# Optimization experiments

Hardware: AMD Instinct MI355X
Metric: run time of the kernel (lower is better)

## Reference

```python
import jax, jax.numpy as jnp
import numpy as np

T, B, DIM, N = 2048, 16, 1024, 64


def setup_inputs() -> dict:
    key = jax.random.key(0)
    ks = jax.random.split(key, 6)
    # xavier-uniform-ish scale for [N, DIM] linear weights
    lim = float(np.sqrt(6.0 / (DIM + N)))
    mk = lambda k: jax.random.uniform(k, (N, DIM), jnp.float32, -lim, lim)
    return {
        "x": jax.random.normal(ks[0], (T, B, DIM), jnp.float32),
        "S": jnp.zeros((B, N, N), jnp.float32),
        "W_k": mk(ks[1]),
        "W_v": mk(ks[2]),
        "W_q": mk(ks[3]),
        "W_alpha": mk(ks[4]),
        "d_alpha": jnp.full((N,), 0.1, jnp.float32),
        "b_alpha": jnp.full((N,), 2.0, jnp.float32),
    }


def reference(x, S, W_k, W_v, W_q, W_alpha, d_alpha, b_alpha):
    # Projections for the whole sequence at once: [T, B, N]
    k_all = jnp.einsum('tbd,nd->tbn', x, W_k)
    v_all = jnp.einsum('tbd,nd->tbn', x, W_v)
    q_all = jnp.einsum('tbd,nd->tbn', x, W_q)
    a_all = jnp.einsum('tbd,nd->tbn', x, W_alpha)

    def step(S, inp):
        k, v, q, ax = inp  # each [B, N]
        retrieved = jnp.einsum('bij,bj->bi', S, k)                 # [B, N]
        alpha = jax.nn.sigmoid(ax + d_alpha * retrieved + b_alpha)  # [B, N]
        outer_vk = v[:, :, None] * k[:, None, :]                    # [B, N, N]
        S = alpha[:, :, None] * S + (1.0 - alpha[:, :, None]) * outer_vk
        out = jnp.einsum('bij,bj->bi', S, q)                        # [B, N]
        out = out * jax.nn.silu(out)
        return S, out

    S_final, output = jax.lax.scan(step, S, (k_all, v_all, q_all, a_all))
    return output, S_final
```

## Files before the change

kernel.cpp:

```cpp
#include <hip/hip_runtime.h>
#include <hip/hip_bf16.h>

#define T_STEPS 2048
#define BATCH 16
#define DIM 1024
#define NDIM 64
#define M_TOTAL (T_STEPS * BATCH)
#define STRIDE (BATCH * NDIM)
#define CH 32

typedef __attribute__((ext_vector_type(8))) short bf16x8;
typedef __attribute__((ext_vector_type(4))) float f32x4;

__device__ inline unsigned pk_bf(float lo, float hi) {
    __hip_bfloat162 h = __float22bfloat162_rn(float2{lo, hi});
    return *(unsigned*)&h;
}

template <int CTRL>
__device__ inline float dpp_add(float x) {
    int v = __builtin_amdgcn_update_dpp(0, __float_as_int(x), CTRL, 0xF, 0xF, true);
    return x + __int_as_float(v);
}
__device__ inline float red16(float x) {
    x = dpp_add<0xB1>(x);
    x = dpp_add<0x4E>(x);
    x = dpp_add<0x141>(x);
    x = dpp_add<0x140>(x);
    return x;
}
__device__ inline float fast_sigmoid(float z) {
    return __builtin_amdgcn_rcpf(1.f + __expf(-z));
}

#define AS1 __attribute__((address_space(1)))
#define AS3 __attribute__((address_space(3)))
__device__ inline void gl_lds16(const float* g, float* l) {
    __builtin_amdgcn_global_load_lds((const AS1 unsigned*)g, (AS3 unsigned*)l, 16, 0, 0);
}
__device__ inline void gl_lds4(const float* g, float* l) {
    __builtin_amdgcn_global_load_lds((const AS1 unsigned*)g, (AS3 unsigned*)l, 4, 0, 0);
}
#define WAIT_VM0 do { __builtin_amdgcn_s_waitcnt(0x0F70); asm volatile("" ::: "memory"); } while (0)

__global__ __launch_bounds__(256, 2) void proj_kernel(
    const float* __restrict__ x,
    const float* __restrict__ Wk, const float* __restrict__ Wv,
    const float* __restrict__ Wq, const float* __restrict__ Wa,
    const float* __restrict__ ba,
    float* __restrict__ outBase, float* __restrict__ kqOut) {
    const int LDA = 40;
    __shared__ unsigned short lA[64 * 40];
    __shared__ unsigned short lB[256 * 40];

    int m0 = blockIdx.x * 64;
    int tid = threadIdx.x;
    int wave = tid >> 6;
    int lane = tid & 63;
    int lrow = lane & 15;
    int quad = lane >> 4;

    f32x4 acc[16];
#pragma unroll
    for (int b = 0; b < 16; b++) acc[b] = (f32x4)(0.f);

    int arow = tid >> 2;
    int acol = (tid & 3) * 8;
    int widx = tid >> 6;
    const float* Wsel = (widx == 0) ? Wk : (widx == 1) ? Wv : (widx == 2) ? Wq : Wa;
    const float* wrow = Wsel + (size_t)(tid & 63) * DIM;
    const float* xrow = x + (size_t)(m0 + arow) * DIM + acol;

    float4 a0 = ((const float4*)xrow)[0], a1 = ((const float4*)xrow)[1];
    float4 bb[8];
#pragma unroll
    for (int jj = 0; jj < 8; jj++) bb[jj] = ((const float4*)wrow)[jj];
    unsigned apk[4], bpk[16];
    apk[0] = pk_bf(a0.x, a0.y); apk[1] = pk_bf(a0.z, a0.w);
    apk[2] = pk_bf(a1.x, a1.y); apk[3] = pk_bf(a1.z, a1.w);
#pragma unroll
    for (int jj = 0; jj < 8; jj++) {
        bpk[2 * jj] = pk_bf(bb[jj].x, bb[jj].y);
        bpk[2 * jj + 1] = pk_bf(bb[jj].z, bb[jj].w);
    }

    for (int k0 = 0; k0 < DIM; k0 += 32) {
        __syncthreads();
        *(uint4*)&lA[arow * LDA + acol] = *(uint4*)&apk[0];
        *(uint4*)&lB[tid * LDA + 0]  = *(uint4*)&bpk[0];
        *(uint4*)&lB[tid * LDA + 8]  = *(uint4*)&bpk[4];
        *(uint4*)&lB[tid * LDA + 16] = *(uint4*)&bpk[8];
        *(uint4*)&lB[tid * LDA + 24] = *(uint4*)&bpk[12];
        __syncthreads();

        bool more = (k0 + 32) < DIM;
        float4 na0, na1, nb[8];
        if (more) {
            const float4* pa = (const float4*)(xrow + k0 + 32);
            na0 = pa[0]; na1 = pa[1];
            const float4* pb = (const float4*)(wrow + k0 + 32);
#pragma unroll
            for (int jj = 0; jj < 8; jj++) nb[jj] = pb[jj];
        }

        bf16x8 af = *(const bf16x8*)&lA[(wave * 16 + lrow) * LDA + quad * 8];
#pragma unroll
        for (int bt = 0; bt < 16; bt++) {
            bf16x8 bfr = *(const bf16x8*)&lB[(bt * 16 + lrow) * LDA + quad * 8];
            acc[bt] = __builtin_amdgcn_mfma_f32_16x16x32_bf16(af, bfr, acc[bt], 0, 0, 0);
        }

        if (more) {
            apk[0] = pk_bf(na0.x, na0.y); apk[1] = pk_bf(na0.z, na0.w);
            apk[2] = pk_bf(na1.x, na1.y); apk[3] = pk_bf(na1.z, na1.w);
#pragma unroll
            for (int jj = 0; jj < 8; jj++) {
                bpk[2 * jj] = pk_bf(nb[jj].x, nb[jj].y);
                bpk[2 * jj + 1] = pk_bf(nb[jj].z, nb[jj].w);
            }
        }
    }

#pragma unroll
    for (int bt = 12; bt < 16; bt++) {
        float bav = ba[(bt - 12) * 16 + lrow];
#pragma unroll
        for (int reg = 0; reg < 4; reg++) acc[bt][reg] += bav;
    }
    const size_t per = (size_t)M_TOTAL * NDIM;
#pragma unroll
    for (int bt = 0; bt < 16; bt++) {
        int n = bt * 16 + lrow;
        float* outW = outBase + (size_t)(n >> 6) * per + (n & 63);
#pragma unroll
        for (int reg = 0; reg < 4; reg++) {
            int m = m0 + wave * 16 + quad * 4 + reg;
            outW[(size_t)m * NDIM] = acc[bt][reg];
        }
    }
#pragma unroll
    for (int reg = 0; reg < 4; reg++) {
        float p = acc[0][reg] * acc[8][reg] + acc[1][reg] * acc[9][reg] +
                  acc[2][reg] * acc[10][reg] + acc[3][reg] * acc[11][reg];
        p = red16(p);
        if (lrow == 0) kqOut[m0 + wave * 16 + quad * 4 + reg] = p;
    }
}

__global__ __launch_bounds__(64, 1) void recur_kernel(
    const float* __restrict__ Kp, const float* __restrict__ Vp,
    const float* __restrict__ Qp, const float* __restrict__ Ap,
    const float* __restrict__ KQp, const float* __restrict__ S0,
    const float* __restrict__ d_alpha, float* __restrict__ out,
    float* __restrict__ Sout) {
    __shared__ float Kl[2][CH][64];
    __shared__ float Ql[2][CH][64];
    __shared__ float VAl[2][CH][8];
    __shared__ float KQl[2][64];

    int b = blockIdx.y;
    int g = blockIdx.x;
    int lane = threadIdx.x;
    int r = lane >> 4;
    int c = lane & 15;
    int i = g * 4 + r;
    int c4 = c * 4;

    float4 s = *(const float4*)(S0 + ((size_t)b * NDIM + i) * NDIM + c4);
    float da = d_alpha[i];

    const float* Kbase = Kp + (size_t)b * NDIM + (size_t)(lane >> 4) * STRIDE + (lane & 15) * 4;
    const float* Qbase = Qp + (size_t)b * NDIM + (size_t)(lane >> 4) * STRIDE + (lane & 15) * 4;
    const float* VAbase = ((lane & 1) ? Ap : Vp) + (size_t)b * NDIM + g * 4 + (size_t)(lane >> 1) * STRIDE;
    const float* KQbase = KQp + b + (size_t)(lane & 31) * BATCH;

    auto load_chunk = [&](int t0, int buf) {
#pragma unroll
        for (int j = 0; j < 8; ++j) {
            gl_lds16(Kbase + (size_t)(t0 + j * 4) * STRIDE, &Kl[buf][j * 4][0]);
            gl_lds16(Qbase + (size_t)(t0 + j * 4) * STRIDE, &Ql[buf][j * 4][0]);
        }
        gl_lds16(VAbase + (size_t)t0 * STRIDE, &VAl[buf][0][0]);
        gl_lds4(KQbase + (size_t)t0 * BATCH, &KQl[buf][0]);
    };

    load_chunk(0, 0);
    WAIT_VM0;

    float* ob = out + (size_t)b * NDIM + i;

    for (int j = 0; j < T_STEPS / CH; ++j) {
        int cb = j & 1;
        if (j < T_STEPS / CH - 1) load_chunk((j + 1) * CH, cb ^ 1);

        const float* Kb = &Kl[cb][0][0];
        const float* Qb = &Ql[cb][0][0];
        const float* Vb = &VAl[cb][0][0];
        const float* Qk = &KQl[cb][0];

        float4 kr[2], qr[2];
        float vr[2], ar[2], kqr[2];
#pragma unroll
        for (int u = 0; u < 2; ++u) {
            kr[u] = *(const float4*)(Kb + u * 64 + c4);
            qr[u] = *(const float4*)(Qb + u * 64 + c4);
            vr[u] = Vb[u * 8 + r];
            ar[u] = Vb[u * 8 + 4 + r];
            kqr[u] = Qk[u];
        }

#pragma unroll
        for (int tl = 0; tl < CH; ++tl) {
            int sl = tl & 1;
            float4 k = kr[sl], q = qr[sl];
            float v = vr[sl], aa = ar[sl], kq = kqr[sl];
            if (tl < CH - 2) {
                kr[sl] = *(const float4*)(Kb + (tl + 2) * 64 + c4);
                qr[sl] = *(const float4*)(Qb + (tl + 2) * 64 + c4);
                vr[sl] = Vb[(tl + 2) * 8 + r];
                ar[sl] = Vb[(tl + 2) * 8 + 4 + r];
                kqr[sl] = Qk[tl + 2];
            }

            float rk = fmaf(k.y, s.y, k.x * s.x) + fmaf(k.w, s.w, k.z * s.z);
            float rq = fmaf(q.y, s.y, q.x * s.x) + fmaf(q.w, s.w, q.z * s.z);
            rk = red16(rk);
            rq = red16(rq);

            float z = fmaf(da, rk, aa);
            float alpha = fast_sigmoid(z);
            float u1 = (1.f - alpha) * v;

            s.x = fmaf(alpha, s.x, u1 * k.x);
            s.y = fmaf(alpha, s.y, u1 * k.y);
            s.z = fmaf(alpha, s.z, u1 * k.z);
            s.w = fmaf(alpha, s.w, u1 * k.w);

            float o = fmaf(alpha, rq, u1 * kq);
            float ov = o * o * fast_sigmoid(o);
            if (c == 0) ob[(size_t)(j * CH + tl) * STRIDE] = ov;
        }
        WAIT_VM0;
    }

    *(float4*)(Sout + ((size_t)b * NDIM + i) * NDIM + c4) = s;
}

extern "C" void kernel_launch(void* const* d_in, const int* in_sizes, int n_in,
                              void* d_out, int out_size, void* d_ws, size_t ws_size,
                              hipStream_t stream) {
    const float* x  = (const float*)d_in[0];
    const float* S0 = (const float*)d_in[1];
    const float* Wk = (const float*)d_in[2];
    const float* Wv = (const float*)d_in[3];
    const float* Wq = (const float*)d_in[4];
    const float* Wa = (const float*)d_in[5];
    const float* da = (const float*)d_in[6];
    const float* ba = (const float*)d_in[7];

    float* out = (float*)d_out;
    float* Sout = out + (size_t)T_STEPS * BATCH * NDIM;

    float* proj = (float*)d_ws;
    const size_t per = (size_t)M_TOTAL * NDIM;
    float* Kp = proj;
    float* Vp = proj + per;
    float* Qp = proj + 2 * per;
    float* Ap = proj + 3 * per;
    float* kq = proj + 4 * per;

    proj_kernel<<<dim3(M_TOTAL / 64), dim3(256), 0, stream>>>(x, Wk, Wv, Wq, Wa, ba, proj, kq);
    recur_kernel<<<dim3(16, BATCH), dim3(64), 0, stream>>>(Kp, Vp, Qp, Ap, kq, S0, da, out, Sout);
}
```

Baseline: 546.8 us.

## Prepack weights to bf16, drop LDS in projection GEMM, widen recurrence rows per lane

Adds a pre-pass that converts the four weight matrices to bf16 once per call. The projection GEMM then reads A and B fragments straight from global memory, with no LDS staging and no barriers, and each wave computes two 16-row tiles that share the same B fragments. The recurrence kernel now gives each lane 8 state columns instead of 4, which halves the block count, shortens the DPP reduction to 8 lanes, and uses packed float2 math for the state update. The trade is more global traffic and less latency hiding in the GEMM, and more serial work per lane in the recurrence, in exchange for fewer reduction steps and fewer barriers.

```diff
diff --git a/kernel.cpp b/kernel.cpp
--- a/kernel.cpp
+++ b/kernel.cpp
@@ -11,6 +11,7 @@
 
 typedef __attribute__((ext_vector_type(8))) short bf16x8;
 typedef __attribute__((ext_vector_type(4))) float f32x4;
+typedef __attribute__((ext_vector_type(2))) float f32x2;
 
 __device__ inline unsigned pk_bf(float lo, float hi) {
     __hip_bfloat162 h = __float22bfloat162_rn(float2{lo, hi});
@@ -29,6 +30,12 @@
     x = dpp_add<0x140>(x);
     return x;
 }
+__device__ inline float red8(float x) {
+    x = dpp_add<0xB1>(x);
+    x = dpp_add<0x4E>(x);
+    x = dpp_add<0x141>(x);
+    return x;
+}
 __device__ inline float fast_sigmoid(float z) {
     return __builtin_amdgcn_rcpf(1.f + __expf(-z));
 }
@@ -43,81 +50,59 @@
 }
 #define WAIT_VM0 do { __builtin_amdgcn_s_waitcnt(0x0F70); asm volatile("" ::: "memory"); } while (0)
 
-__global__ __launch_bounds__(256, 2) void proj_kernel(
-    const float* __restrict__ x,
+__global__ __launch_bounds__(256) void pack_w(
     const float* __restrict__ Wk, const float* __restrict__ Wv,
     const float* __restrict__ Wq, const float* __restrict__ Wa,
+    unsigned short* __restrict__ Wb) {
+    int n = blockIdx.x;
+    int sel = n >> 6;
+    const float* W = (sel == 0) ? Wk : (sel == 1) ? Wv : (sel == 2) ? Wq : Wa;
+    int k4 = threadIdx.x * 4;
+    float4 f = *(const float4*)(W + (size_t)(n & 63) * DIM + k4);
+    uint2 u;
+    u.x = pk_bf(f.x, f.y);
+    u.y = pk_bf(f.z, f.w);
+    *(uint2*)(Wb + (size_t)n * DIM + k4) = u;
+}
+
+__global__ __launch_bounds__(256, 2) void proj_kernel(
+    const float* __restrict__ x, const unsigned short* __restrict__ Wb,
     const float* __restrict__ ba,
     float* __restrict__ outBase, float* __restrict__ kqOut) {
-    const int LDA = 40;
-    __shared__ unsigned short lA[64 * 40];
-    __shared__ unsigned short lB[256 * 40];
-
-    int m0 = blockIdx.x * 64;
     int tid = threadIdx.x;
-    int wave = tid >> 6;
+    int wv = tid >> 6;
     int lane = tid & 63;
     int lrow = lane & 15;
     int quad = lane >> 4;
-
-    f32x4 acc[16];
-#pragma unroll
-    for (int b = 0; b < 16; b++) acc[b] = (f32x4)(0.f);
-
-    int arow = tid >> 2;
-    int acol = (tid & 3) * 8;
-    int widx = tid >> 6;
-    const float* Wsel = (widx == 0) ? Wk : (widx == 1) ? Wv : (widx == 2) ? Wq : Wa;
-    const float* wrow = Wsel + (size_t)(tid & 63) * DIM;
-    const float* xrow = x + (size_t)(m0 + arow) * DIM + acol;
-
-    float4 a0 = ((const float4*)xrow)[0], a1 = ((const float4*)xrow)[1];
-    float4 bb[8];
-#pragma unroll
-    for (int jj = 0; jj < 8; jj++) bb[jj] = ((const float4*)wrow)[jj];
-    unsigned apk[4], bpk[16];
-    apk[0] = pk_bf(a0.x, a0.y); apk[1] = pk_bf(a0.z, a0.w);
-    apk[2] = pk_bf(a1.x, a1.y); apk[3] = pk_bf(a1.z, a1.w);
-#pragma unroll
-    for (int jj = 0; jj < 8; jj++) {
-        bpk[2 * jj] = pk_bf(bb[jj].x, bb[jj].y);
-        bpk[2 * jj + 1] = pk_bf(bb[jj].z, bb[jj].w);
-    }
+    int m0 = blockIdx.x * 128 + wv * 32;
+
+    f32x4 acc[2][16];
+#pragma unroll
+    for (int a = 0; a < 2; a++)
+#pragma unroll
+        for (int b = 0; b < 16; b++) acc[a][b] = (f32x4)(0.f);
+
+    const float* xr0 = x + (size_t)(m0 + lrow) * DIM + quad * 8;
+    const float* xr1 = xr0 + (size_t)16 * DIM;
+    const unsigned short* wb = Wb + (size_t)lrow * DIM + quad * 8;
 
     for (int k0 = 0; k0 < DIM; k0 += 32) {
-        __syncthreads();
-        *(uint4*)&lA[arow * LDA + acol] = *(uint4*)&apk[0];
-        *(uint4*)&lB[tid * LDA + 0]  = *(uint4*)&bpk[0];
-        *(uint4*)&lB[tid * LDA + 8]  = *(uint4*)&bpk[4];
-        *(uint4*)&lB[tid * LDA + 16] = *(uint4*)&bpk[8];
-        *(uint4*)&lB[tid * LDA + 24] = *(uint4*)&bpk[12];
-        __syncthreads();
-
-        bool more = (k0 + 32) < DIM;
-        float4 na0, na1, nb[8];
-        if (more) {
-            const float4* pa = (const float4*)(xrow + k0 + 32);
-            na0 = pa[0]; na1 = pa[1];
-            const float4* pb = (const float4*)(wrow + k0 + 32);
-#pragma unroll
-            for (int jj = 0; jj < 8; jj++) nb[jj] = pb[jj];
-        }
-
-        bf16x8 af = *(const bf16x8*)&lA[(wave * 16 + lrow) * LDA + quad * 8];
+        float4 a00 = ((const float4*)(xr0 + k0))[0];
+        float4 a01 = ((const float4*)(xr0 + k0))[1];
+        float4 a10 = ((const float4*)(xr1 + k0))[0];
+        float4 a11 = ((const float4*)(xr1 + k0))[1];
+        unsigned p0[4], p1[4];
+        p0[0] = pk_bf(a00.x, a00.y); p0[1] = pk_bf(a00.z, a00.w);
+        p0[2] = pk_bf(a01.x, a01.y); p0[3] = pk_bf(a01.z, a01.w);
+        p1[0] = pk_bf(a10.x, a10.y); p1[1] = pk_bf(a10.z, a10.w);
+        p1[2] = pk_bf(a11.x, a11.y); p1[3] = pk_bf(a11.z, a11.w);
+        bf16x8 af0 = *(bf16x8*)&p0[0];
+        bf16x8 af1 = *(bf16x8*)&p1[0];
 #pragma unroll
         for (int bt = 0; bt < 16; bt++) {
-            bf16x8 bfr = *(const bf16x8*)&lB[(bt * 16 + lrow) * LDA + quad * 8];
-            acc[bt] = __builtin_amdgcn_mfma_f32_16x16x32_bf16(af, bfr, acc[bt], 0, 0, 0);
-        }
-
-        if (more) {
-            apk[0] = pk_bf(na0.x, na0.y); apk[1] = pk_bf(na0.z, na0.w);
-            apk[2] = pk_bf(na1.x, na1.y); apk[3] = pk_bf(na1.z, na1.w);
-#pragma unroll
-            for (int jj = 0; jj < 8; jj++) {
-                bpk[2 * jj] = pk_bf(nb[jj].x, nb[jj].y);
-                bpk[2 * jj + 1] = pk_bf(nb[jj].z, nb[jj].w);
-            }
+            bf16x8 bfr = *(const bf16x8*)(wb + (size_t)(bt * 16) * DIM + k0);
+            acc[0][bt] = __builtin_amdgcn_mfma_f32_16x16x32_bf16(af0, bfr, acc[0][bt], 0, 0, 0);
+            acc[1][bt] = __builtin_amdgcn_mfma_f32_16x16x32_bf16(af1, bfr, acc[1][bt], 0, 0, 0);
         }
     }
 
@@ -125,26 +110,32 @@
     for (int bt = 12; bt < 16; bt++) {
         float bav = ba[(bt - 12) * 16 + lrow];
 #pragma unroll
-        for (int reg = 0; reg < 4; reg++) acc[bt][reg] += bav;
+        for (int rt = 0; rt < 2; rt++)
+#pragma unroll
+            for (int reg = 0; reg < 4; reg++) acc[rt][bt][reg] += bav;
     }
     const size_t per = (size_t)M_TOTAL * NDIM;
 #pragma unroll
-    for (int bt = 0; bt < 16; bt++) {
-        int n = bt * 16 + lrow;
-        float* outW = outBase + (size_t)(n >> 6) * per + (n & 63);
+    for (int rt = 0; rt < 2; rt++)
+#pragma unroll
+        for (int bt = 0; bt < 16; bt++) {
+            int n = bt * 16 + lrow;
+            float* outW = outBase + (size_t)(n >> 6) * per + (n & 63);
+#pragma unroll
+            for (int reg = 0; reg < 4; reg++) {
+                int m = m0 + rt * 16 + quad * 4 + reg;
+                outW[(size_t)m * NDIM] = acc[rt][bt][reg];
+            }
+        }
+#pragma unroll
+    for (int rt = 0; rt < 2; rt++)
 #pragma unroll
         for (int reg = 0; reg < 4; reg++) {
-            int m = m0 + wave * 16 + quad * 4 + reg;
-            outW[(size_t)m * NDIM] = acc[bt][reg];
-        }
-    }
-#pragma unroll
-    for (int reg = 0; reg < 4; reg++) {
-        float p = acc[0][reg] * acc[8][reg] + acc[1][reg] * acc[9][reg] +
-                  acc[2][reg] * acc[10][reg] + acc[3][reg] * acc[11][reg];
-        p = red16(p);
-        if (lrow == 0) kqOut[m0 + wave * 16 + quad * 4 + reg] = p;
-    }
+            float p = acc[rt][0][reg] * acc[rt][8][reg] + acc[rt][1][reg] * acc[rt][9][reg] +
+                      acc[rt][2][reg] * acc[rt][10][reg] + acc[rt][3][reg] * acc[rt][11][reg];
+            p = red16(p);
+            if (lrow == 0) kqOut[m0 + rt * 16 + quad * 4 + reg] = p;
+        }
 }
 
 __global__ __launch_bounds__(64, 1) void recur_kernel(
@@ -155,23 +146,26 @@
     float* __restrict__ Sout) {
     __shared__ float Kl[2][CH][64];
     __shared__ float Ql[2][CH][64];
-    __shared__ float VAl[2][CH][8];
+    __shared__ float VAl[2][CH][16];
     __shared__ float KQl[2][64];
 
     int b = blockIdx.y;
     int g = blockIdx.x;
     int lane = threadIdx.x;
-    int r = lane >> 4;
-    int c = lane & 15;
-    int i = g * 4 + r;
-    int c4 = c * 4;
-
-    float4 s = *(const float4*)(S0 + ((size_t)b * NDIM + i) * NDIM + c4);
+    int rg = lane >> 3;
+    int c = lane & 7;
+    int i = g * 8 + rg;
+    int c8 = c * 8;
+
+    const float* sp = S0 + ((size_t)b * NDIM + i) * NDIM + c8;
+    float4 sA = ((const float4*)sp)[0], sB = ((const float4*)sp)[1];
+    f32x2 s0 = {sA.x, sA.y}, s1 = {sA.z, sA.w}, s2 = {sB.x, sB.y}, s3 = {sB.z, sB.w};
     float da = d_alpha[i];
 
     const float* Kbase = Kp + (size_t)b * NDIM + (size_t)(lane >> 4) * STRIDE + (lane & 15) * 4;
     const float* Qbase = Qp + (size_t)b * NDIM + (size_t)(lane >> 4) * STRIDE + (lane & 15) * 4;
-    const float* VAbase = ((lane & 1) ? Ap : Vp) + (size_t)b * NDIM + g * 4 + (size_t)(lane >> 1) * STRIDE;
+    const float* VAbase = ((lane & 2) ? Ap : Vp) + (size_t)b * NDIM + g * 8 + (lane & 1) * 4 +
+                          (size_t)(lane >> 2) * STRIDE;
     const float* KQbase = KQp + b + (size_t)(lane & 31) * BATCH;
 
     auto load_chunk = [&](int t0, int buf) {
@@ -181,6 +175,7 @@
             gl_lds16(Qbase + (size_t)(t0 + j * 4) * STRIDE, &Ql[buf][j * 4][0]);
         }
         gl_lds16(VAbase + (size_t)t0 * STRIDE, &VAl[buf][0][0]);
+        gl_lds16(VAbase + (size_t)(t0 + 16) * STRIDE, &VAl[buf][16][0]);
         gl_lds4(KQbase + (size_t)t0 * BATCH, &KQl[buf][0]);
     };
 
@@ -191,59 +186,47 @@
 
     for (int j = 0; j < T_STEPS / CH; ++j) {
         int cb = j & 1;
-        if (j < T_STEPS / CH - 1) load_chunk((j + 1) * CH, cb ^ 1);
+        if (j + 1 < T_STEPS / CH) load_chunk((j + 1) * CH, cb ^ 1);
 
         const float* Kb = &Kl[cb][0][0];
         const float* Qb = &Ql[cb][0][0];
         const float* Vb = &VAl[cb][0][0];
         const float* Qk = &KQl[cb][0];
 
-        float4 kr[2], qr[2];
-        float vr[2], ar[2], kqr[2];
-#pragma unroll
-        for (int u = 0; u < 2; ++u) {
-            kr[u] = *(const float4*)(Kb + u * 64 + c4);
-            qr[u] = *(const float4*)(Qb + u * 64 + c4);
-            vr[u] = Vb[u * 8 + r];
-            ar[u] = Vb[u * 8 + 4 + r];
-            kqr[u] = Qk[u];
-        }
-
 #pragma unroll
         for (int tl = 0; tl < CH; ++tl) {
-            int sl = tl & 1;
-            float4 k = kr[sl], q = qr[sl];
-            float v = vr[sl], aa = ar[sl], kq = kqr[sl];
-            if (tl < CH - 2) {
-                kr[sl] = *(const float4*)(Kb + (tl + 2) * 64 + c4);
-                qr[sl] = *(const float4*)(Qb + (tl + 2) * 64 + c4);
-                vr[sl] = Vb[(tl + 2) * 8 + r];
-                ar[sl] = Vb[(tl + 2) * 8 + 4 + r];
-                kqr[sl] = Qk[tl + 2];
-            }
-
-            float rk = fmaf(k.y, s.y, k.x * s.x) + fmaf(k.w, s.w, k.z * s.z);
-            float rq = fmaf(q.y, s.y, q.x * s.x) + fmaf(q.w, s.w, q.z * s.z);
-            rk = red16(rk);
-            rq = red16(rq);
-
-            float z = fmaf(da, rk, aa);
-            float alpha = fast_sigmoid(z);
-            float u1 = (1.f - alpha) * v;
-
-            s.x = fmaf(alpha, s.x, u1 * k.x);
-            s.y = fmaf(alpha, s.y, u1 * k.y);
-            s.z = fmaf(alpha, s.z, u1 * k.z);
-            s.w = fmaf(alpha, s.w, u1 * k.w);
-
-            float o = fmaf(alpha, rq, u1 * kq);
+            const f32x2* kp2 = (const f32x2*)(Kb + tl * 64 + c8);
+            f32x2 k0 = kp2[0], k1 = kp2[1], k2 = kp2[2], k3 = kp2[3];
+            const f32x2* qp2 = (const f32x2*)(Qb + tl * 64 + c8);
+            f32x2 q0 = qp2[0], q1 = qp2[1], q2 = qp2[2], q3 = qp2[3];
+            float v = Vb[tl * 16 + rg];
+            float aa = Vb[tl * 16 + 8 + rg];
+            float kq = Qk[tl];
+
+            f32x2 pk_ = (k0 * s0 + k1 * s1) + (k2 * s2 + k3 * s3);
+            f32x2 pq_ = (q0 * s0 + q1 * s1) + (q2 * s2 + q3 * s3);
+            float rk = red8(pk_.x + pk_.y);
+            float rq = red8(pq_.x + pq_.y);
+
+            float alpha = fast_sigmoid(fmaf(da, rk, aa));
+            float oma = 1.f - alpha;
+
+            f32x2 w0 = v * k0, w1 = v * k1, w2 = v * k2, w3 = v * k3;
+            s0 = w0 + alpha * (s0 - w0);
+            s1 = w1 + alpha * (s1 - w1);
+            s2 = w2 + alpha * (s2 - w2);
+            s3 = w3 + alpha * (s3 - w3);
+
+            float o = fmaf(alpha, rq, oma * v * kq);
             float ov = o * o * fast_sigmoid(o);
             if (c == 0) ob[(size_t)(j * CH + tl) * STRIDE] = ov;
         }
         WAIT_VM0;
     }
 
-    *(float4*)(Sout + ((size_t)b * NDIM + i) * NDIM + c4) = s;
+    float* so = Sout + ((size_t)b * NDIM + i) * NDIM + c8;
+    ((float4*)so)[0] = float4{s0.x, s0.y, s1.x, s1.y};
+    ((float4*)so)[1] = float4{s2.x, s2.y, s3.x, s3.y};
 }
 
 extern "C" void kernel_launch(void* const* d_in, const int* in_sizes, int n_in,
@@ -261,14 +244,16 @@
     float* out = (float*)d_out;
     float* Sout = out + (size_t)T_STEPS * BATCH * NDIM;
 
+    const size_t per = (size_t)M_TOTAL * NDIM;
     float* proj = (float*)d_ws;
-    const size_t per = (size_t)M_TOTAL * NDIM;
     float* Kp = proj;
     float* Vp = proj + per;
     float* Qp = proj + 2 * per;
     float* Ap = proj + 3 * per;
     float* kq = proj + 4 * per;
-
-    proj_kernel<<<dim3(M_TOTAL / 64), dim3(256), 0, stream>>>(x, Wk, Wv, Wq, Wa, ba, proj, kq);
-    recur_kernel<<<dim3(16, BATCH), dim3(64), 0, stream>>>(Kp, Vp, Qp, Ap, kq, S0, da, out, Sout);
-}
+    unsigned short* Wb = (unsigned short*)(kq + M_TOTAL);
+
+    pack_w<<<dim3(256), dim3(256), 0, stream>>>(Wk, Wv, Wq, Wa, Wb);
+    proj_kernel<<<dim3(M_TOTAL / 128), dim3(256), 0, stream>>>(x, Wb, ba, proj, kq);
+    recur_kernel<<<dim3(8, BATCH), dim3(64), 0, stream>>>(Kp, Vp, Qp, Ap, kq, S0, da, out, Sout);
+}
```

Result: slower. 742.4 us (+35.8%).
